# Performance work log

Measured on AMD Instinct MI355X. Metric: run time of the kernel, lower is better.

## Reference

```python
import jax, jax.numpy as jnp
import numpy as np

B, S, D, H = 4, 2048, 512, 8
DEPTH = D // H
BAND = 16  # log_thresholds [1,2,4,8,16] union == distance <= 16


def setup_inputs() -> dict:
    key = jax.random.key(0)
    ks = jax.random.split(key, 11)
    sc = 0.02
    return {
        "q": jax.random.normal(ks[0], (B, S, D), jnp.float32),
        "k": jax.random.normal(ks[1], (B, S, D), jnp.float32),
        "v": jax.random.normal(ks[2], (B, S, D), jnp.float32),
        "wq": jax.random.normal(ks[3], (D, D), jnp.float32) * sc,
        "bq": jnp.zeros((D,), jnp.float32),
        "wk": jax.random.normal(ks[4], (D, D), jnp.float32) * sc,
        "bk": jnp.zeros((D,), jnp.float32),
        "wv": jax.random.normal(ks[5], (D, D), jnp.float32) * sc,
        "bv": jnp.zeros((D,), jnp.float32),
        "wo": jax.random.normal(ks[6], (D, D), jnp.float32) * sc,
        "bo": jnp.zeros((D,), jnp.float32),
    }


def _split_heads(x):
    # [B,S,D] -> [B,H,S,depth]
    b, s, _ = x.shape
    return x.reshape(b, s, H, DEPTH).transpose(0, 2, 1, 3)


def reference(q, k, v, wq, bq, wk, bk, wv, bv, wo, bo):
    qh = _split_heads(q @ wq + bq)
    kh = _split_heads(k @ wk + bk)
    vh = _split_heads(v @ wv + bv)
    scale = 1.0 / jnp.sqrt(jnp.float32(DEPTH))
    logits = jnp.einsum("bhqd,bhkd->bhqk", qh, kh) * scale  # [B,H,S,S]
    idx = jnp.arange(S)
    keep = jnp.abs(idx[:, None] - idx[None, :]) <= BAND  # band mask [S,S]
    logits = jnp.where(keep[None, None], logits, jnp.float32(-1e9))
    attn = jax.nn.softmax(logits, axis=-1)
    out = jnp.einsum("bhqk,bhkd->bhqd", attn, vh)
    out = out.transpose(0, 2, 1, 3).reshape(q.shape[0], -1, D)
    return out @ wo + bo
```

## Files before the change

### kernel.cpp

```cpp
#include <hip/hip_runtime.h>

typedef unsigned int uint;
typedef unsigned short ushort;
typedef __attribute__((ext_vector_type(8))) short bf16x8;
typedef __attribute__((ext_vector_type(4))) float f32x4;

namespace {
constexpr int kS = 2048;
constexpr int kD = 512;
constexpr int kH = 8;
constexpr int kBand = 16;
}

static __device__ __forceinline__ ushort f2bf(float f) {
  uint u = __builtin_bit_cast(uint, f);
  u = (u + 0x7fffu + ((u >> 16) & 1u)) >> 16;
  return (ushort)u;
}

static __device__ __forceinline__ bf16x8 cvt8(f32x4 lo, f32x4 hi) {
  uint4 r;
  asm("v_cvt_pk_bf16_f32 %0, %1, %2" : "=v"(r.x) : "v"(lo[0]), "v"(lo[1]));
  asm("v_cvt_pk_bf16_f32 %0, %1, %2" : "=v"(r.y) : "v"(lo[2]), "v"(lo[3]));
  asm("v_cvt_pk_bf16_f32 %0, %1, %2" : "=v"(r.z) : "v"(hi[0]), "v"(hi[1]));
  asm("v_cvt_pk_bf16_f32 %0, %1, %2" : "=v"(r.w) : "v"(hi[2]), "v"(hi[3]));
  return __builtin_bit_cast(bf16x8, r);
}

#define GLD16(gp, lp)                                                   \
  __builtin_amdgcn_global_load_lds(                                     \
      (const __attribute__((address_space(1))) uint*)(gp),              \
      (__attribute__((address_space(3))) uint*)(lp), 16, 0, 0)

#define FENCE asm volatile("" ::: "memory")

__global__ __launch_bounds__(256) void prep_kernel(
    const float* __restrict__ wq, const float* __restrict__ wk,
    const float* __restrict__ wv, const float* __restrict__ wo,
    ushort* __restrict__ WT) {
  __shared__ float Ws[64][65];
  const int w = blockIdx.x;
  const int tid = threadIdx.x;
  const int z = w >> 6;
  const float* W = z == 0 ? wq : (z == 1 ? wk : (z == 2 ? wv : wo));
  ushort* T = WT + (size_t)z * kD * kD;
  const int kt = ((w >> 3) & 7) * 64, nt = (w & 7) * 64;
  const int r = tid >> 2, c0 = (tid & 3) * 16;
#pragma unroll
  for (int i = 0; i < 4; ++i) {
    const float4 x =
        *(const float4*)(W + (size_t)(kt + r) * kD + nt + c0 + i * 4);
    Ws[r][c0 + i * 4 + 0] = x.x;
    Ws[r][c0 + i * 4 + 1] = x.y;
    Ws[r][c0 + i * 4 + 2] = x.z;
    Ws[r][c0 + i * 4 + 3] = x.w;
  }
  __syncthreads();
  const int n = tid >> 2, k0 = (tid & 3) * 16;
  alignas(16) ushort tmp[16];
#pragma unroll
  for (int i = 0; i < 16; ++i) tmp[i] = f2bf(Ws[k0 + i][n]);
  ushort* dst = T + (size_t)(nt + n) * kD + kt + k0;
  *(uint4*)(dst + 0) = *(const uint4*)&tmp[0];
  *(uint4*)(dst + 8) = *(const uint4*)&tmp[8];
}

__global__ __launch_bounds__(256, 3) void gemm_qkv(
    const float* __restrict__ q, const float* __restrict__ k,
    const float* __restrict__ v, const ushort* __restrict__ WT,
    const float* __restrict__ bq, const float* __restrict__ bk,
    const float* __restrict__ bv, ushort* __restrict__ Qp,
    ushort* __restrict__ Kp, ushort* __restrict__ VT) {
  const int mode = blockIdx.z;
  const float* Ab = mode == 0 ? q : (mode == 1 ? k : v);
  const float* bias = mode == 0 ? bq : (mode == 1 ? bk : bv);
  const ushort* BT = WT + (size_t)mode * kD * kD;

  constexpr int A_STAGE = 128 * 32;
  constexpr int B_BASE = 3 * A_STAGE;
  __shared__ alignas(16) ushort smem[B_BASE + 12288];

  const int tid = threadIdx.x;
  const int wave = tid >> 6, lane = tid & 63, l15 = lane & 15, qd = lane >> 4;
  const int wm = (wave >> 1) * 64, wn = (wave & 1) * 64;
  const int lin = blockIdx.x;
  const int xcd = lin & 7, j = lin >> 3;
  const int rblk = xcd + 8 * (j >> 2), cblk = j & 3;
  const int row0 = rblk * 128, col0 = cblk * 128;
  const int sw = (l15 & 3) ^ (l15 >> 2);

  const int ar = tid >> 1;
  const int acp = (tid & 1) * 2;
  const int as_ = (ar & 3) ^ ((ar >> 2) & 3);
  const float* pAg = Ab + (size_t)(row0 + ar) * kD + acp * 8;
  const uint wA0 = (uint)(ar * 32 + ((acp ^ as_) * 8));
  const uint wA1 = (uint)(ar * 32 + (((acp + 1) ^ as_) * 8));

  const ushort* pB[2];
  uint ldsB[2];
#pragma unroll
  for (int i = 0; i < 2; ++i) {
    const int linear = i * 256 + tid;
    const int r = linear >> 2, c = linear & 3;
    const int g = c ^ ((r & 3) ^ ((r >> 2) & 3));
    pB[i] = BT + (size_t)(col0 + r) * kD + g * 8;
    ldsB[i] = (uint)B_BASE + (uint)(i * 256 + wave * 64) * 8;
  }

  f32x4 areg[2][4];
#define LOADA(slot, kk)                                               \
  { _Pragma("unroll") for (int c = 0; c < 4; ++c)                     \
      areg[slot][c] = *(const f32x4*)(pAg + (kk) + c * 4); }
#define WRITEA(st, slot)                                              \
  {                                                                   \
    *(bf16x8*)&smem[(st) * A_STAGE + wA0] =                           \
        cvt8(areg[slot][0], areg[slot][1]);                           \
    *(bf16x8*)&smem[(st) * A_STAGE + wA1] =                           \
        cvt8(areg[slot][2], areg[slot][3]);                           \
  }
#define ISSUEB(kk, st)                                                \
  { _Pragma("unroll") for (int i = 0; i < 2; ++i)                     \
      GLD16(pB[i] + (kk), &smem[ldsB[i] + (st) * 4096]); }

  f32x4 acc[4][4];
#pragma unroll
  for (int mi = 0; mi < 4; ++mi)
#pragma unroll
    for (int ni = 0; ni < 4; ++ni) acc[mi][ni] = (f32x4)(0.f);

  LOADA(0, 0);
  FENCE;
  ISSUEB(0, 0);
  FENCE;
  LOADA(1, 32);
  FENCE;
  ISSUEB(32, 1);
  FENCE;
  WRITEA(0, 0);

#pragma unroll
  for (int it = 0; it < 16; ++it) {
    if (it < 15) {
      WRITEA((it + 1) % 3, (it + 1) & 1);
      if (it < 14) LOADA(it & 1, (it + 2) * 32);
      asm volatile("s_waitcnt lgkmcnt(0)\n\ts_barrier" ::: "memory");
      if (it < 14) ISSUEB((it + 2) * 32, (it + 2) % 3);
      FENCE;
    } else {
      asm volatile("s_waitcnt vmcnt(0) lgkmcnt(0)\n\ts_barrier" ::: "memory");
    }
    const ushort* as2 = &smem[(it % 3) * A_STAGE];
    const ushort* bs = &smem[B_BASE + (it % 3) * 4096];
    bf16x8 af[4], br[4];
#pragma unroll
    for (int mi = 0; mi < 4; ++mi)
      af[mi] = *(const bf16x8*)&as2[(wm + mi * 16 + l15) * 32 + (qd ^ sw) * 8];
#pragma unroll
    for (int ni = 0; ni < 4; ++ni)
      br[ni] = *(const bf16x8*)&bs[(wn + ni * 16 + l15) * 32 + (qd ^ sw) * 8];
#pragma unroll
    for (int mi = 0; mi < 4; ++mi)
#pragma unroll
      for (int ni = 0; ni < 4; ++ni)
        acc[mi][ni] = __builtin_amdgcn_mfma_f32_16x16x32_bf16(
            af[mi], br[ni], acc[mi][ni], 0, 0, 0);
  }
#undef LOADA
#undef WRITEA
#undef ISSUEB

  float bcol[4];
#pragma unroll
  for (int ni = 0; ni < 4; ++ni) bcol[ni] = bias[col0 + wn + ni * 16 + l15];

  __syncthreads();

  ushort* T = &smem[wave * 4608];
  if (mode <= 1) {
#pragma unroll
    for (int mi = 0; mi < 4; ++mi)
#pragma unroll
      for (int ni = 0; ni < 4; ++ni)
#pragma unroll
        for (int r = 0; r < 4; ++r)
          T[(mi * 16 + qd * 4 + r) * 72 + ni * 16 + l15] =
              f2bf(acc[mi][ni][r] + bcol[ni]);
  } else {
#pragma unroll
    for (int mi = 0; mi < 4; ++mi)
#pragma unroll
      for (int ni = 0; ni < 4; ++ni)
#pragma unroll
        for (int r = 0; r < 4; ++r)
          T[(ni * 16 + l15) * 72 + mi * 16 + qd * 4 + r] =
              f2bf(acc[mi][ni][r] + bcol[ni]);
  }
  asm volatile("s_waitcnt lgkmcnt(0)" ::: "memory");

  const ushort* Trow = &smem[wave * 4608 + lane * 72];
  if (mode <= 1) {
    ushort* C = (mode == 0) ? Qp : Kp;
    ushort* dst = C + (size_t)(row0 + wm + lane) * kD + col0 + wn;
#pragma unroll
    for (int c = 0; c < 8; ++c)
      *(uint4*)(dst + c * 8) = *(const uint4*)(Trow + c * 8);
  } else {
    const int n_g = col0 + wn + lane;
    const int h = n_g >> 6, d = n_g & 63;
    const int t0 = row0 + wm;
    const int b = t0 >> 11, ss = t0 & (kS - 1);
    ushort* dst = VT + ((size_t)(b * kH + h) * 64 + d) * kS + ss;
#pragma unroll
    for (int c = 0; c < 8; ++c)
      *(uint4*)(dst + c * 8) = *(const uint4*)(Trow + c * 8);
  }
}

__global__ __launch_bounds__(64, 2) void attn_kernel(
    const ushort* __restrict__ Qp, const ushort* __restrict__ Kp,
    const ushort* __restrict__ VT, ushort* __restrict__ Ob) {
  __shared__ alignas(16) ushort Pl[32 * 72];

  const int lane = threadIdx.x, l15 = lane & 15, qd = lane >> 4;
  const int bh = blockIdx.y, b = bh >> 3, h = bh & 7;
  const int q0 = blockIdx.x * 32;
  const int colA = h * 64;

  bf16x8 qf[2][2], kf[4][2];
#pragma unroll
  for (int mi = 0; mi < 2; ++mi) {
    const size_t base =
        ((size_t)b * kS + q0 + mi * 16 + l15) * kD + colA + qd * 8;
#pragma unroll
    for (int kc = 0; kc < 2; ++kc)
      qf[mi][kc] = *(const bf16x8*)&Qp[base + kc * 32];
  }
#pragma unroll
  for (int ni = 0; ni < 4; ++ni) {
    int key = q0 - kBand + ni * 16 + l15;
    key = key < 0 ? 0 : (key > kS - 1 ? kS - 1 : key);
    const size_t base = ((size_t)b * kS + key) * kD + colA + qd * 8;
#pragma unroll
    for (int kc = 0; kc < 2; ++kc)
      kf[ni][kc] = *(const bf16x8*)&Kp[base + kc * 32];
  }

  f32x4 S[2][4];
#pragma unroll
  for (int mi = 0; mi < 2; ++mi)
#pragma unroll
    for (int ni = 0; ni < 4; ++ni) S[mi][ni] = (f32x4)(0.f);
#pragma unroll
  for (int mi = 0; mi < 2; ++mi)
#pragma unroll
    for (int ni = 0; ni < 4; ++ni)
#pragma unroll
      for (int kc = 0; kc < 2; ++kc)
        S[mi][ni] = __builtin_amdgcn_mfma_f32_16x16x32_bf16(
            qf[mi][kc], kf[ni][kc], S[mi][ni], 0, 0, 0);

#pragma unroll
  for (int mi = 0; mi < 2; ++mi)
#pragma unroll
    for (int ni = 0; ni < 4; ++ni)
#pragma unroll
      for (int r = 0; r < 4; ++r) {
        const int q_local = mi * 16 + qd * 4 + r;
        const int key_local = ni * 16 + l15;
        const int key = q0 - kBand + key_local;
        const int dlt = key_local - q_local;
        const bool ok = (dlt >= 0) && (dlt <= 32) && (key >= 0) && (key < kS);
        S[mi][ni][r] = ok ? S[mi][ni][r] * 0.125f : -3.0e38f;
      }

  float inv[2][4];
#pragma unroll
  for (int mi = 0; mi < 2; ++mi)
#pragma unroll
    for (int r = 0; r < 4; ++r) {
      float m = S[mi][0][r];
#pragma unroll
      for (int ni = 1; ni < 4; ++ni) m = fmaxf(m, S[mi][ni][r]);
      m = fmaxf(m, __shfl_xor(m, 1));
      m = fmaxf(m, __shfl_xor(m, 2));
      m = fmaxf(m, __shfl_xor(m, 4));
      m = fmaxf(m, __shfl_xor(m, 8));
      float s = 0.f;
#pragma unroll
      for (int ni = 0; ni < 4; ++ni) {
        const float e = __expf(S[mi][ni][r] - m);
        S[mi][ni][r] = e;
        s += e;
      }
      s += __shfl_xor(s, 1);
      s += __shfl_xor(s, 2);
      s += __shfl_xor(s, 4);
      s += __shfl_xor(s, 8);
      inv[mi][r] = 1.f / s;
    }

#pragma unroll
  for (int mi = 0; mi < 2; ++mi)
#pragma unroll
    for (int ni = 0; ni < 4; ++ni)
#pragma unroll
      for (int r = 0; r < 4; ++r)
        Pl[(mi * 16 + qd * 4 + r) * 72 + ni * 16 + l15] = f2bf(S[mi][ni][r]);
  __syncthreads();

  f32x4 O[2][4];
#pragma unroll
  for (int mi = 0; mi < 2; ++mi)
#pragma unroll
    for (int nt = 0; nt < 4; ++nt) O[mi][nt] = (f32x4)(0.f);

#pragma unroll
  for (int kc = 0; kc < 2; ++kc) {
    bf16x8 pf[2], vfr[4];
#pragma unroll
    for (int mi = 0; mi < 2; ++mi)
      pf[mi] = *(const bf16x8*)&Pl[(mi * 16 + l15) * 72 + kc * 32 + qd * 8];
    int kb0 = q0 - kBand + kc * 32 + qd * 8;
    kb0 = kb0 < 0 ? 0 : (kb0 > kS - 8 ? kS - 8 : kb0);
#pragma unroll
    for (int nt = 0; nt < 4; ++nt)
      vfr[nt] =
          *(const bf16x8*)&VT[((size_t)bh * 64 + nt * 16 + l15) * kS + kb0];
#pragma unroll
    for (int mi = 0; mi < 2; ++mi)
#pragma unroll
      for (int nt = 0; nt < 4; ++nt)
        O[mi][nt] = __builtin_amdgcn_mfma_f32_16x16x32_bf16(pf[mi], vfr[nt],
                                                            O[mi][nt], 0, 0, 0);
  }

#pragma unroll
  for (int mi = 0; mi < 2; ++mi)
#pragma unroll
    for (int nt = 0; nt < 4; ++nt)
#pragma unroll
      for (int r = 0; r < 4; ++r)
        Pl[(mi * 16 + qd * 4 + r) * 72 + nt * 16 + l15] =
            f2bf(O[mi][nt][r] * inv[mi][r]);
  asm volatile("s_waitcnt lgkmcnt(0)" ::: "memory");

  const int row = lane >> 1, half = lane & 1;
  ushort* dst = Ob + ((size_t)b * kS + q0 + row) * kD + colA + half * 32;
  const ushort* Trow = &Pl[row * 72 + half * 32];
#pragma unroll
  for (int c = 0; c < 4; ++c)
    *(uint4*)(dst + c * 8) = *(const uint4*)(Trow + c * 8);
}

__global__ __launch_bounds__(256) void gemm_out(
    const ushort* __restrict__ Ab, const ushort* __restrict__ BT,
    const float* __restrict__ bias, float* __restrict__ outp) {
  constexpr int A_STAGE = 64 * 32;
  constexpr int B_BASE = 3 * A_STAGE;
  __shared__ alignas(16) ushort smem[B_BASE + 12288];

  const int tid = threadIdx.x;
  const int wave = tid >> 6, lane = tid & 63, l15 = lane & 15, qd = lane >> 4;
  const int wn = wave * 32;
  const int lin = blockIdx.x;
  const int xcd = lin & 7, j = lin >> 3;
  const int rblk = xcd + 8 * (j >> 2), cblk = j & 3;
  const int row0 = rblk * 64, col0 = cblk * 128;
  const int sw = (l15 & 3) ^ (l15 >> 2);

  const ushort* pA0;
  uint ldsA0;
  {
    const int r = tid >> 2, c = tid & 3;
    const int g = c ^ ((r & 3) ^ ((r >> 2) & 3));
    pA0 = Ab + (size_t)(row0 + r) * kD + g * 8;
    ldsA0 = (uint)(wave * 64) * 8;
  }
  const ushort* pB[2];
  uint ldsB[2];
#pragma unroll
  for (int i = 0; i < 2; ++i) {
    const int linear = i * 256 + tid;
    const int r = linear >> 2, c = linear & 3;
    const int g = c ^ ((r & 3) ^ ((r >> 2) & 3));
    pB[i] = BT + (size_t)(col0 + r) * kD + g * 8;
    ldsB[i] = (uint)B_BASE + (uint)(i * 256 + wave * 64) * 8;
  }

#define ISSUE3(kk, st)                                                \
  {                                                                   \
    GLD16(pA0 + (kk), &smem[ldsA0 + (st) * A_STAGE]);                 \
    _Pragma("unroll") for (int i = 0; i < 2; ++i)                     \
        GLD16(pB[i] + (kk), &smem[ldsB[i] + (st) * 4096]);            \
  }

  f32x4 acc[4][2];
#pragma unroll
  for (int mi = 0; mi < 4; ++mi)
#pragma unroll
    for (int ni = 0; ni < 2; ++ni) acc[mi][ni] = (f32x4)(0.f);

  ISSUE3(0, 0);
  ISSUE3(32, 1);
#pragma unroll
  for (int it = 0; it < 16; ++it) {
    if (it < 15)
      asm volatile("s_waitcnt vmcnt(3) lgkmcnt(0)\n\ts_barrier" ::: "memory");
    else
      asm volatile("s_waitcnt vmcnt(0) lgkmcnt(0)\n\ts_barrier" ::: "memory");
    if (it < 14) ISSUE3((it + 2) * 32, (it + 2) % 3);
    const ushort* as2 = &smem[(it % 3) * A_STAGE];
    const ushort* bs = &smem[B_BASE + (it % 3) * 4096];
    bf16x8 af[4], br[2];
#pragma unroll
    for (int mi = 0; mi < 4; ++mi)
      af[mi] = *(const bf16x8*)&as2[(mi * 16 + l15) * 32 + (qd ^ sw) * 8];
#pragma unroll
    for (int ni = 0; ni < 2; ++ni)
      br[ni] = *(const bf16x8*)&bs[(wn + ni * 16 + l15) * 32 + (qd ^ sw) * 8];
#pragma unroll
    for (int mi = 0; mi < 4; ++mi)
#pragma unroll
      for (int ni = 0; ni < 2; ++ni)
        acc[mi][ni] = __builtin_amdgcn_mfma_f32_16x16x32_bf16(
            af[mi], br[ni], acc[mi][ni], 0, 0, 0);
  }
#undef ISSUE3

#pragma unroll
  for (int ni = 0; ni < 2; ++ni) {
    const int n_g = col0 + wn + ni * 16 + l15;
    const float bc = bias[n_g];
#pragma unroll
    for (int mi = 0; mi < 4; ++mi)
#pragma unroll
      for (int r = 0; r < 4; ++r) {
        const int token = row0 + mi * 16 + qd * 4 + r;
        outp[(size_t)token * kD + n_g] = acc[mi][ni][r] + bc;
      }
  }
}

extern "C" void kernel_launch(void* const* d_in, const int* in_sizes, int n_in,
                              void* d_out, int out_size, void* d_ws,
                              size_t ws_size, hipStream_t stream) {
  const float* q = (const float*)d_in[0];
  const float* k = (const float*)d_in[1];
  const float* v = (const float*)d_in[2];
  const float* wq = (const float*)d_in[3];
  const float* bq = (const float*)d_in[4];
  const float* wk = (const float*)d_in[5];
  const float* bk = (const float*)d_in[6];
  const float* wv = (const float*)d_in[7];
  const float* bv = (const float*)d_in[8];
  const float* wo = (const float*)d_in[9];
  const float* bo = (const float*)d_in[10];
  float* out = (float*)d_out;

  const size_t n1 = (size_t)8192 * kD;
  ushort* Qp = (ushort*)d_ws;
  ushort* Kp = Qp + n1;
  ushort* VT = Kp + n1;
  ushort* Ob = VT + n1;
  ushort* WT = Ob + n1;

  prep_kernel<<<dim3(256), 256, 0, stream>>>(wq, wk, wv, wo, WT);
  gemm_qkv<<<dim3(256, 1, 3), 256, 0, stream>>>(q, k, v, WT, bq, bk, bv, Qp,
                                                Kp, VT);
  attn_kernel<<<dim3(kS / 32, 32), 64, 0, stream>>>(Qp, Kp, VT, Ob);
  gemm_out<<<dim3(512), 256, 0, stream>>>(Ob, WT + (size_t)3 * kD * kD, bo,
                                          out);
}
```

Before: 161.6 us.

## Replace LDS-staged GEMMs with single-wave direct-from-global register-prefetch GEMMs

Both projection GEMMs drop the multi-wave, LDS-staged, triple-buffered tiles. Instead, each single 64-thread wavefront computes a 64x64 output tile and loads its MFMA operands straight from global memory into registers, prefetching one k-step ahead. This removes the barriers and LDS traffic and spreads the work over many more small blocks. In exchange, operands are no longer shared between waves through LDS, so each wave re-reads A and B from global or L2. The fp32 q/k/v inputs are also converted to bf16 by every wave that reads them.

```diff
diff --git a/kernel.cpp b/kernel.cpp
--- a/kernel.cpp
+++ b/kernel.cpp
@@ -26,13 +26,6 @@
   asm("v_cvt_pk_bf16_f32 %0, %1, %2" : "=v"(r.w) : "v"(hi[2]), "v"(hi[3]));
   return __builtin_bit_cast(bf16x8, r);
 }
-
-#define GLD16(gp, lp)                                                   \
-  __builtin_amdgcn_global_load_lds(                                     \
-      (const __attribute__((address_space(1))) uint*)(gp),              \
-      (__attribute__((address_space(3))) uint*)(lp), 16, 0, 0)
-
-#define FENCE asm volatile("" ::: "memory")
 
 __global__ __launch_bounds__(256) void prep_kernel(
     const float* __restrict__ wq, const float* __restrict__ wk,
@@ -65,62 +58,34 @@
   *(uint4*)(dst + 8) = *(const uint4*)&tmp[8];
 }
 
-__global__ __launch_bounds__(256, 3) void gemm_qkv(
+__global__ __launch_bounds__(64) void gemm_qkv(
     const float* __restrict__ q, const float* __restrict__ k,
     const float* __restrict__ v, const ushort* __restrict__ WT,
     const float* __restrict__ bq, const float* __restrict__ bk,
     const float* __restrict__ bv, ushort* __restrict__ Qp,
     ushort* __restrict__ Kp, ushort* __restrict__ VT) {
-  const int mode = blockIdx.z;
+  __shared__ alignas(16) ushort Tl[64 * 72];
+
+  const int lane = threadIdx.x, l15 = lane & 15, qd = lane >> 4;
+  const int lin = blockIdx.x;
+  const int xcd = lin & 7, j = lin >> 3;
+  const int rlin = xcd + 8 * (j >> 3);
+  const int col = (j & 7) * 64;
+  const int mode = rlin >> 7;
+  const int row0 = (rlin & 127) * 64;
+
   const float* Ab = mode == 0 ? q : (mode == 1 ? k : v);
   const float* bias = mode == 0 ? bq : (mode == 1 ? bk : bv);
   const ushort* BT = WT + (size_t)mode * kD * kD;
 
-  constexpr int A_STAGE = 128 * 32;
-  constexpr int B_BASE = 3 * A_STAGE;
-  __shared__ alignas(16) ushort smem[B_BASE + 12288];
-
-  const int tid = threadIdx.x;
-  const int wave = tid >> 6, lane = tid & 63, l15 = lane & 15, qd = lane >> 4;
-  const int wm = (wave >> 1) * 64, wn = (wave & 1) * 64;
-  const int lin = blockIdx.x;
-  const int xcd = lin & 7, j = lin >> 3;
-  const int rblk = xcd + 8 * (j >> 2), cblk = j & 3;
-  const int row0 = rblk * 128, col0 = cblk * 128;
-  const int sw = (l15 & 3) ^ (l15 >> 2);
-
-  const int ar = tid >> 1;
-  const int acp = (tid & 1) * 2;
-  const int as_ = (ar & 3) ^ ((ar >> 2) & 3);
-  const float* pAg = Ab + (size_t)(row0 + ar) * kD + acp * 8;
-  const uint wA0 = (uint)(ar * 32 + ((acp ^ as_) * 8));
-  const uint wA1 = (uint)(ar * 32 + (((acp + 1) ^ as_) * 8));
-
-  const ushort* pB[2];
-  uint ldsB[2];
-#pragma unroll
-  for (int i = 0; i < 2; ++i) {
-    const int linear = i * 256 + tid;
-    const int r = linear >> 2, c = linear & 3;
-    const int g = c ^ ((r & 3) ^ ((r >> 2) & 3));
-    pB[i] = BT + (size_t)(col0 + r) * kD + g * 8;
-    ldsB[i] = (uint)B_BASE + (uint)(i * 256 + wave * 64) * 8;
-  }
-
-  f32x4 areg[2][4];
-#define LOADA(slot, kk)                                               \
-  { _Pragma("unroll") for (int c = 0; c < 4; ++c)                     \
-      areg[slot][c] = *(const f32x4*)(pAg + (kk) + c * 4); }
-#define WRITEA(st, slot)                                              \
-  {                                                                   \
-    *(bf16x8*)&smem[(st) * A_STAGE + wA0] =                           \
-        cvt8(areg[slot][0], areg[slot][1]);                           \
-    *(bf16x8*)&smem[(st) * A_STAGE + wA1] =                           \
-        cvt8(areg[slot][2], areg[slot][3]);                           \
-  }
-#define ISSUEB(kk, st)                                                \
-  { _Pragma("unroll") for (int i = 0; i < 2; ++i)                     \
-      GLD16(pB[i] + (kk), &smem[ldsB[i] + (st) * 4096]); }
+  const float* pAm[4];
+  const ushort* pBn[4];
+#pragma unroll
+  for (int mi = 0; mi < 4; ++mi)
+    pAm[mi] = Ab + (size_t)(row0 + mi * 16 + l15) * kD + qd * 8;
+#pragma unroll
+  for (int ni = 0; ni < 4; ++ni)
+    pBn[ni] = BT + (size_t)(col + ni * 16 + l15) * kD + qd * 8;
 
   f32x4 acc[4][4];
 #pragma unroll
@@ -128,54 +93,45 @@
 #pragma unroll
     for (int ni = 0; ni < 4; ++ni) acc[mi][ni] = (f32x4)(0.f);
 
-  LOADA(0, 0);
-  FENCE;
-  ISSUEB(0, 0);
-  FENCE;
-  LOADA(1, 32);
-  FENCE;
-  ISSUEB(32, 1);
-  FENCE;
-  WRITEA(0, 0);
+  f32x4 an[8];
+  bf16x8 bn[4];
+#pragma unroll
+  for (int mi = 0; mi < 4; ++mi) {
+    an[2 * mi] = *(const f32x4*)(pAm[mi]);
+    an[2 * mi + 1] = *(const f32x4*)(pAm[mi] + 4);
+  }
+#pragma unroll
+  for (int ni = 0; ni < 4; ++ni) bn[ni] = *(const bf16x8*)(pBn[ni]);
 
 #pragma unroll
   for (int it = 0; it < 16; ++it) {
+    bf16x8 af[4], bu[4];
+#pragma unroll
+    for (int mi = 0; mi < 4; ++mi) af[mi] = cvt8(an[2 * mi], an[2 * mi + 1]);
+#pragma unroll
+    for (int ni = 0; ni < 4; ++ni) bu[ni] = bn[ni];
     if (it < 15) {
-      WRITEA((it + 1) % 3, (it + 1) & 1);
-      if (it < 14) LOADA(it & 1, (it + 2) * 32);
-      asm volatile("s_waitcnt lgkmcnt(0)\n\ts_barrier" ::: "memory");
-      if (it < 14) ISSUEB((it + 2) * 32, (it + 2) % 3);
-      FENCE;
-    } else {
-      asm volatile("s_waitcnt vmcnt(0) lgkmcnt(0)\n\ts_barrier" ::: "memory");
+      const int kk = (it + 1) * 32;
+#pragma unroll
+      for (int mi = 0; mi < 4; ++mi) {
+        an[2 * mi] = *(const f32x4*)(pAm[mi] + kk);
+        an[2 * mi + 1] = *(const f32x4*)(pAm[mi] + kk + 4);
+      }
+#pragma unroll
+      for (int ni = 0; ni < 4; ++ni) bn[ni] = *(const bf16x8*)(pBn[ni] + kk);
     }
-    const ushort* as2 = &smem[(it % 3) * A_STAGE];
-    const ushort* bs = &smem[B_BASE + (it % 3) * 4096];
-    bf16x8 af[4], br[4];
-#pragma unroll
-    for (int mi = 0; mi < 4; ++mi)
-      af[mi] = *(const bf16x8*)&as2[(wm + mi * 16 + l15) * 32 + (qd ^ sw) * 8];
-#pragma unroll
-    for (int ni = 0; ni < 4; ++ni)
-      br[ni] = *(const bf16x8*)&bs[(wn + ni * 16 + l15) * 32 + (qd ^ sw) * 8];
 #pragma unroll
     for (int mi = 0; mi < 4; ++mi)
 #pragma unroll
       for (int ni = 0; ni < 4; ++ni)
         acc[mi][ni] = __builtin_amdgcn_mfma_f32_16x16x32_bf16(
-            af[mi], br[ni], acc[mi][ni], 0, 0, 0);
-  }
-#undef LOADA
-#undef WRITEA
-#undef ISSUEB
+            af[mi], bu[ni], acc[mi][ni], 0, 0, 0);
+  }
 
   float bcol[4];
 #pragma unroll
-  for (int ni = 0; ni < 4; ++ni) bcol[ni] = bias[col0 + wn + ni * 16 + l15];
-
-  __syncthreads();
-
-  ushort* T = &smem[wave * 4608];
+  for (int ni = 0; ni < 4; ++ni) bcol[ni] = bias[col + ni * 16 + l15];
+
   if (mode <= 1) {
 #pragma unroll
     for (int mi = 0; mi < 4; ++mi)
@@ -183,7 +139,7 @@
       for (int ni = 0; ni < 4; ++ni)
 #pragma unroll
         for (int r = 0; r < 4; ++r)
-          T[(mi * 16 + qd * 4 + r) * 72 + ni * 16 + l15] =
+          Tl[(mi * 16 + qd * 4 + r) * 72 + ni * 16 + l15] =
               f2bf(acc[mi][ni][r] + bcol[ni]);
   } else {
 #pragma unroll
@@ -192,23 +148,22 @@
       for (int ni = 0; ni < 4; ++ni)
 #pragma unroll
         for (int r = 0; r < 4; ++r)
-          T[(ni * 16 + l15) * 72 + mi * 16 + qd * 4 + r] =
+          Tl[(ni * 16 + l15) * 72 + mi * 16 + qd * 4 + r] =
               f2bf(acc[mi][ni][r] + bcol[ni]);
   }
   asm volatile("s_waitcnt lgkmcnt(0)" ::: "memory");
 
-  const ushort* Trow = &smem[wave * 4608 + lane * 72];
+  const ushort* Trow = &Tl[lane * 72];
   if (mode <= 1) {
     ushort* C = (mode == 0) ? Qp : Kp;
-    ushort* dst = C + (size_t)(row0 + wm + lane) * kD + col0 + wn;
+    ushort* dst = C + (size_t)(row0 + lane) * kD + col;
 #pragma unroll
     for (int c = 0; c < 8; ++c)
       *(uint4*)(dst + c * 8) = *(const uint4*)(Trow + c * 8);
   } else {
-    const int n_g = col0 + wn + lane;
+    const int n_g = col + lane;
     const int h = n_g >> 6, d = n_g & 63;
-    const int t0 = row0 + wm;
-    const int b = t0 >> 11, ss = t0 & (kS - 1);
+    const int b = row0 >> 11, ss = row0 & (kS - 1);
     ushort* dst = VT + ((size_t)(b * kH + h) * 64 + d) * kS + ss;
 #pragma unroll
     for (int c = 0; c < 8; ++c)
@@ -352,84 +307,61 @@
     *(uint4*)(dst + c * 8) = *(const uint4*)(Trow + c * 8);
 }
 
-__global__ __launch_bounds__(256) void gemm_out(
+__global__ __launch_bounds__(64) void gemm_out(
     const ushort* __restrict__ Ab, const ushort* __restrict__ BT,
     const float* __restrict__ bias, float* __restrict__ outp) {
-  constexpr int A_STAGE = 64 * 32;
-  constexpr int B_BASE = 3 * A_STAGE;
-  __shared__ alignas(16) ushort smem[B_BASE + 12288];
-
-  const int tid = threadIdx.x;
-  const int wave = tid >> 6, lane = tid & 63, l15 = lane & 15, qd = lane >> 4;
-  const int wn = wave * 32;
+  const int lane = threadIdx.x, l15 = lane & 15, qd = lane >> 4;
   const int lin = blockIdx.x;
   const int xcd = lin & 7, j = lin >> 3;
-  const int rblk = xcd + 8 * (j >> 2), cblk = j & 3;
-  const int row0 = rblk * 64, col0 = cblk * 128;
-  const int sw = (l15 & 3) ^ (l15 >> 2);
-
-  const ushort* pA0;
-  uint ldsA0;
-  {
-    const int r = tid >> 2, c = tid & 3;
-    const int g = c ^ ((r & 3) ^ ((r >> 2) & 3));
-    pA0 = Ab + (size_t)(row0 + r) * kD + g * 8;
-    ldsA0 = (uint)(wave * 64) * 8;
-  }
-  const ushort* pB[2];
-  uint ldsB[2];
-#pragma unroll
-  for (int i = 0; i < 2; ++i) {
-    const int linear = i * 256 + tid;
-    const int r = linear >> 2, c = linear & 3;
-    const int g = c ^ ((r & 3) ^ ((r >> 2) & 3));
-    pB[i] = BT + (size_t)(col0 + r) * kD + g * 8;
-    ldsB[i] = (uint)B_BASE + (uint)(i * 256 + wave * 64) * 8;
-  }
-
-#define ISSUE3(kk, st)                                                \
-  {                                                                   \
-    GLD16(pA0 + (kk), &smem[ldsA0 + (st) * A_STAGE]);                 \
-    _Pragma("unroll") for (int i = 0; i < 2; ++i)                     \
-        GLD16(pB[i] + (kk), &smem[ldsB[i] + (st) * 4096]);            \
-  }
-
-  f32x4 acc[4][2];
+  const int row0 = (xcd + 8 * (j >> 3)) * 64;
+  const int col = (j & 7) * 64;
+
+  const ushort* pAm[4];
+  const ushort* pBn[4];
 #pragma unroll
   for (int mi = 0; mi < 4; ++mi)
-#pragma unroll
-    for (int ni = 0; ni < 2; ++ni) acc[mi][ni] = (f32x4)(0.f);
-
-  ISSUE3(0, 0);
-  ISSUE3(32, 1);
+    pAm[mi] = Ab + (size_t)(row0 + mi * 16 + l15) * kD + qd * 8;
+#pragma unroll
+  for (int ni = 0; ni < 4; ++ni)
+    pBn[ni] = BT + (size_t)(col + ni * 16 + l15) * kD + qd * 8;
+
+  f32x4 acc[4][4];
+#pragma unroll
+  for (int mi = 0; mi < 4; ++mi)
+#pragma unroll
+    for (int ni = 0; ni < 4; ++ni) acc[mi][ni] = (f32x4)(0.f);
+
+  bf16x8 an[4], bn[4];
+#pragma unroll
+  for (int mi = 0; mi < 4; ++mi) an[mi] = *(const bf16x8*)(pAm[mi]);
+#pragma unroll
+  for (int ni = 0; ni < 4; ++ni) bn[ni] = *(const bf16x8*)(pBn[ni]);
+
 #pragma unroll
   for (int it = 0; it < 16; ++it) {
-    if (it < 15)
-      asm volatile("s_waitcnt vmcnt(3) lgkmcnt(0)\n\ts_barrier" ::: "memory");
-    else
-      asm volatile("s_waitcnt vmcnt(0) lgkmcnt(0)\n\ts_barrier" ::: "memory");
-    if (it < 14) ISSUE3((it + 2) * 32, (it + 2) % 3);
-    const ushort* as2 = &smem[(it % 3) * A_STAGE];
-    const ushort* bs = &smem[B_BASE + (it % 3) * 4096];
-    bf16x8 af[4], br[2];
+    bf16x8 af[4], bu[4];
+#pragma unroll
+    for (int mi = 0; mi < 4; ++mi) af[mi] = an[mi];
+#pragma unroll
+    for (int ni = 0; ni < 4; ++ni) bu[ni] = bn[ni];
+    if (it < 15) {
+      const int kk = (it + 1) * 32;
+#pragma unroll
+      for (int mi = 0; mi < 4; ++mi) an[mi] = *(const bf16x8*)(pAm[mi] + kk);
+#pragma unroll
+      for (int ni = 0; ni < 4; ++ni) bn[ni] = *(const bf16x8*)(pBn[ni] + kk);
+    }
 #pragma unroll
     for (int mi = 0; mi < 4; ++mi)
-      af[mi] = *(const bf16x8*)&as2[(mi * 16 + l15) * 32 + (qd ^ sw) * 8];
-#pragma unroll
-    for (int ni = 0; ni < 2; ++ni)
-      br[ni] = *(const bf16x8*)&bs[(wn + ni * 16 + l15) * 32 + (qd ^ sw) * 8];
-#pragma unroll
-    for (int mi = 0; mi < 4; ++mi)
-#pragma unroll
-      for (int ni = 0; ni < 2; ++ni)
+#pragma unroll
+      for (int ni = 0; ni < 4; ++ni)
         acc[mi][ni] = __builtin_amdgcn_mfma_f32_16x16x32_bf16(
-            af[mi], br[ni], acc[mi][ni], 0, 0, 0);
-  }
-#undef ISSUE3
-
-#pragma unroll
-  for (int ni = 0; ni < 2; ++ni) {
-    const int n_g = col0 + wn + ni * 16 + l15;
+            af[mi], bu[ni], acc[mi][ni], 0, 0, 0);
+  }
+
+#pragma unroll
+  for (int ni = 0; ni < 4; ++ni) {
+    const int n_g = col + ni * 16 + l15;
     const float bc = bias[n_g];
 #pragma unroll
     for (int mi = 0; mi < 4; ++mi)
@@ -465,9 +397,8 @@
   ushort* WT = Ob + n1;
 
   prep_kernel<<<dim3(256), 256, 0, stream>>>(wq, wk, wv, wo, WT);
-  gemm_qkv<<<dim3(256, 1, 3), 256, 0, stream>>>(q, k, v, WT, bq, bk, bv, Qp,
-                                                Kp, VT);
+  gemm_qkv<<<dim3(3072), 64, 0, stream>>>(q, k, v, WT, bq, bk, bv, Qp, Kp, VT);
   attn_kernel<<<dim3(kS / 32, 32), 64, 0, stream>>>(Qp, Kp, VT, Ob);
-  gemm_out<<<dim3(512), 256, 0, stream>>>(Ob, WT + (size_t)3 * kD * kD, bo,
+  gemm_out<<<dim3(1024), 64, 0, stream>>>(Ob, WT + (size_t)3 * kD * kD, bo,
                                           out);
 }
```

Result: slower. 208.8 us (+29.2%).
